# Performance work log

Measured on AMD Instinct MI355X. Metric: run time of the kernel, lower is better.

The kernel has to match this reference:

```python
import jax, jax.numpy as jnp
import numpy as np

EMB_DIM = 1024
NUM_HEADS = 16
HEAD_DIM = EMB_DIM // NUM_HEADS
B, S = 4, 1024


def _split_heads(x):
    # [B, S, E] -> [B, H, S, E/H]
    b, s, e = x.shape
    return x.reshape(b, s, NUM_HEADS, e // NUM_HEADS).transpose(0, 2, 1, 3)


def _merge_heads(x):
    # [B, H, S, D] -> [B, S, H*D]
    b, h, s, d = x.shape
    return x.transpose(0, 2, 1, 3).reshape(b, s, h * d)


def setup_inputs() -> dict:
    key = jax.random.key(0)
    ks = jax.random.split(key, 8)
    w_scale = 0.02
    return {
        "Re": jax.random.normal(ks[0], (B, S, EMB_DIM), jnp.float32),
        "Im": jax.random.normal(ks[1], (B, S, EMB_DIM), jnp.float32),
        "pos_enc": jax.random.normal(ks[2], (B, S, HEAD_DIM), jnp.float32),
        "Wq": jax.random.normal(ks[3], (EMB_DIM, EMB_DIM), jnp.float32) * w_scale,
        "bq": jnp.zeros((EMB_DIM,), jnp.float32),
        "Wk": jax.random.normal(ks[4], (EMB_DIM, EMB_DIM), jnp.float32) * w_scale,
        "bk": jnp.zeros((EMB_DIM,), jnp.float32),
        "Wv": jax.random.normal(ks[5], (EMB_DIM, EMB_DIM), jnp.float32) * w_scale,
        "bv": jnp.zeros((EMB_DIM,), jnp.float32),
        "Wo": jax.random.normal(ks[6], (EMB_DIM, EMB_DIM), jnp.float32) * w_scale,
        "bo": jnp.zeros((EMB_DIM,), jnp.float32),
    }


def reference(Re, Im, pos_enc, Wq, bq, Wk, bk, Wv, bv, Wo, bo):
    # projections + head split
    Q = _split_heads(Re @ Wq + bq)          # [B,H,S,D]
    K = _split_heads(Re @ Wk + bk)          # [B,H,S,D]
    ImH = _split_heads(Im)                  # [B,H,S,D]
    P = pos_enc[:, None, :, :]              # [B,1,S,D] broadcast over heads
    Q = Q + P
    K = K + P
    # real part of (Q + i*Im)(K - i*Im)^T = Q K^T + Im Im^T
    denom = jnp.sqrt(jnp.asarray(EMB_DIM, Q.dtype))  # NOTE: sqrt(emb_dim), as in source
    scores = (jnp.einsum("bhqd,bhkd->bhqk", Q, K)
              + jnp.einsum("bhqd,bhkd->bhqk", ImH, ImH)) / denom
    weights = jax.nn.softmax(scores, axis=-1)
    V = _split_heads(Re @ Wv + bv) + P      # value_pos_enc=True
    out = jnp.einsum("bhqk,bhkd->bhqd", weights, V)
    return _merge_heads(out) @ Wo + bo
```

## Files before the change

### kernel.cpp

```cpp
#include <hip/hip_runtime.h>
#include <hip/hip_bf16.h>
#include <stdint.h>

#define BATCH 4
#define SEQ   1024
#define EMB   1024
#define NHEAD 16
#define HDIM  64
#define MTOT  (BATCH*SEQ)
#define MELEM (MTOT*EMB)

typedef __attribute__((ext_vector_type(8))) short short8;
typedef __attribute__((ext_vector_type(4))) float f32x4;
typedef __attribute__((ext_vector_type(4))) unsigned short us4;

static __device__ __forceinline__ unsigned short f2bf_fast(float f) {
  unsigned u = __builtin_bit_cast(unsigned, f);
  return (unsigned short)((u + 0x8000u) >> 16);
}

static __device__ __forceinline__ void cp16(const void* g, const void* lds_uniform) {
  __builtin_amdgcn_global_load_lds(
      (const __attribute__((address_space(1))) unsigned int*)(uintptr_t)g,
      (__attribute__((address_space(3))) unsigned int*)(unsigned int)(uintptr_t)lds_uniform,
      16, 0, 0);
}

__global__ __launch_bounds__(256) void cvt_bf16(const float* __restrict__ in0,
                                                const float* __restrict__ in1,
                                                short* __restrict__ out0,
                                                short* __restrict__ out1) {
  const float* in  = blockIdx.y ? in1  : in0;
  short*       out = blockIdx.y ? out1 : out0;
  int i = blockIdx.x * 256 + threadIdx.x;
  float4 f = ((const float4*)in)[i];
  unsigned r0 = ((unsigned)f2bf_fast(f.y) << 16) | f2bf_fast(f.x);
  unsigned r1 = ((unsigned)f2bf_fast(f.w) << 16) | f2bf_fast(f.z);
  ((uint2*)out)[i] = make_uint2(r0, r1);
}

__global__ __launch_bounds__(256) void wtrans(const float* __restrict__ W0,
                                              const float* __restrict__ W1,
                                              const float* __restrict__ W2,
                                              const float* __restrict__ W3,
                                              short* __restrict__ WtBase) {
  const int z = blockIdx.z;
  const float* W = (z == 0) ? W0 : (z == 1) ? W1 : (z == 2) ? W2 : W3;
  short* Wt = WtBase + (size_t)z * EMB * EMB;
  __shared__ short tile[32][33];
  int nT = blockIdx.x * 32, kT = blockIdx.y * 32;
  int tx = threadIdx.x, ty = threadIdx.y;
  #pragma unroll
  for (int i = 0; i < 4; ++i)
    tile[ty + 8*i][tx] = (short)f2bf_fast(W[(size_t)(kT + ty + 8*i) * EMB + nT + tx]);
  __syncthreads();
  #pragma unroll
  for (int i = 0; i < 4; ++i)
    Wt[(size_t)(nT + ty + 8*i) * EMB + kT + tx] = tile[tx][ty + 8*i];
}

__global__ __launch_bounds__(256) void gemm_qkv(const short* __restrict__ A,
                                                const short* __restrict__ Wt,
                                                const float* __restrict__ bq,
                                                const float* __restrict__ bk,
                                                const float* __restrict__ bv,
                                                const float* __restrict__ pos,
                                                short* __restrict__ QKbase,
                                                short* __restrict__ vtOut) {
  const int m0 = blockIdx.y * 128, n0 = blockIdx.x * 64;
  const int z = n0 >> 10;
  const float* bias = (z == 0) ? bq : (z == 1 ? bk : bv);

  __shared__ __align__(16) short As[128 * 64];
  __shared__ __align__(16) short Bs[64 * 64];

  const int t = threadIdx.x;
  const int lane = t & 63, w = t >> 6;
  const int wm = w >> 1, wn = w & 1;
  const int quad = lane >> 4, l16 = lane & 15;
  const int lrow8 = lane >> 3, lchunk = lane & 7;
  const int gch = lchunk ^ lrow8;
  const int sw7 = l16 & 7;

  const short* Arow = A  + (size_t)(m0 + w * 32 + lrow8) * EMB + gch * 8;
  const short* Brow = Wt + (size_t)(n0 + w * 16 + lrow8) * EMB + gch * 8;

  f32x4 acc[4][2] = {};

  for (int k0 = 0; k0 < EMB; k0 += 64) {
    #pragma unroll
    for (int s = 0; s < 4; ++s)
      cp16(Arow + (size_t)(s * 8) * EMB + k0, &As[(w * 32 + s * 8) * 64]);
    #pragma unroll
    for (int s = 0; s < 2; ++s)
      cp16(Brow + (size_t)(s * 8) * EMB + k0, &Bs[(w * 16 + s * 8) * 64]);
    __syncthreads();
    #pragma unroll
    for (int ks = 0; ks < 2; ++ks) {
      const int chv = ((ks << 2) + quad) ^ sw7;
      short8 af[4], bfr[2];
      #pragma unroll
      for (int i = 0; i < 4; ++i)
        af[i] = *(const short8*)&As[(wm * 64 + i * 16 + l16) * 64 + chv * 8];
      #pragma unroll
      for (int j = 0; j < 2; ++j)
        bfr[j] = *(const short8*)&Bs[(wn * 32 + j * 16 + l16) * 64 + chv * 8];
      #pragma unroll
      for (int i = 0; i < 4; ++i)
        #pragma unroll
        for (int j = 0; j < 2; ++j)
          acc[i][j] = __builtin_amdgcn_mfma_f32_16x16x32_bf16(af[i], bfr[j], acc[i][j], 0, 0, 0);
    }
    __syncthreads();
  }

  #pragma unroll
  for (int i = 0; i < 4; ++i) {
    int mbase = m0 + wm * 64 + i * 16 + quad * 4;
    #pragma unroll
    for (int j = 0; j < 2; ++j) {
      int n = n0 + wn * 32 + j * 16 + l16;
      int nl = n & 1023;
      float bn = bias[nl];
      int d = nl & (HDIM - 1);
      if (z == 2) {
        int bh = (mbase >> 10) * NHEAD + (nl >> 6);
        int s = mbase & (SEQ - 1);
        us4 pk;
        #pragma unroll
        for (int r = 0; r < 4; ++r) {
          float v = acc[i][j][r] + bn + pos[(size_t)(mbase + r) * HDIM + d];
          pk[r] = f2bf_fast(v);
        }
        *(us4*)&vtOut[((size_t)bh * HDIM + d) * SEQ + s] = pk;
      } else {
        #pragma unroll
        for (int r = 0; r < 4; ++r) {
          int mm = mbase + r;
          float v = acc[i][j][r] + bn + pos[(size_t)mm * HDIM + d];
          QKbase[(size_t)z * MELEM + (size_t)mm * EMB + nl] = (short)f2bf_fast(v);
        }
      }
    }
  }
}

__global__ __launch_bounds__(256) void gemm_wo(const short* __restrict__ A,
                                               const short* __restrict__ Bt,
                                               const float* __restrict__ bias,
                                               float* __restrict__ out) {
  const int m0 = blockIdx.y * 64, n0 = blockIdx.x * 64;

  __shared__ __align__(16) short As[64 * 64];
  __shared__ __align__(16) short Bs[64 * 64];

  const int t = threadIdx.x;
  const int lane = t & 63, w = t >> 6;
  const int wm = w >> 1, wn = w & 1;
  const int quad = lane >> 4, l16 = lane & 15;
  const int lrow8 = lane >> 3, lchunk = lane & 7;
  const int gch = lchunk ^ lrow8;
  const int sw7 = l16 & 7;

  const short* Arow = A  + (size_t)(m0 + w * 16 + lrow8) * EMB + gch * 8;
  const short* Brow = Bt + (size_t)(n0 + w * 16 + lrow8) * EMB + gch * 8;

  f32x4 acc[2][2] = {};

  for (int k0 = 0; k0 < EMB; k0 += 64) {
    #pragma unroll
    for (int s = 0; s < 2; ++s) {
      cp16(Arow + (size_t)(s * 8) * EMB + k0, &As[(w * 16 + s * 8) * 64]);
      cp16(Brow + (size_t)(s * 8) * EMB + k0, &Bs[(w * 16 + s * 8) * 64]);
    }
    __syncthreads();
    #pragma unroll
    for (int ks = 0; ks < 2; ++ks) {
      const int chv = ((ks << 2) + quad) ^ sw7;
      short8 af[2], bfr[2];
      #pragma unroll
      for (int i = 0; i < 2; ++i)
        af[i] = *(const short8*)&As[(wm * 32 + i * 16 + l16) * 64 + chv * 8];
      #pragma unroll
      for (int j = 0; j < 2; ++j)
        bfr[j] = *(const short8*)&Bs[(wn * 32 + j * 16 + l16) * 64 + chv * 8];
      #pragma unroll
      for (int i = 0; i < 2; ++i)
        #pragma unroll
        for (int j = 0; j < 2; ++j)
          acc[i][j] = __builtin_amdgcn_mfma_f32_16x16x32_bf16(af[i], bfr[j], acc[i][j], 0, 0, 0);
    }
    __syncthreads();
  }

  #pragma unroll
  for (int i = 0; i < 2; ++i) {
    int mbase = m0 + wm * 32 + i * 16 + quad * 4;
    #pragma unroll
    for (int j = 0; j < 2; ++j) {
      int n = n0 + wn * 32 + j * 16 + l16;
      float bn = bias[n];
      #pragma unroll
      for (int r = 0; r < 4; ++r)
        out[(size_t)(mbase + r) * EMB + n] = acc[i][j][r] + bn;
    }
  }
}

__global__ __launch_bounds__(256) void attn(const short* __restrict__ Qp,
                                            const short* __restrict__ Kp,
                                            const short* __restrict__ VtG,
                                            const short* __restrict__ Imb,
                                            short* __restrict__ attnA) {
  const int qb = blockIdx.y * 64;
  const int bh = blockIdx.x;
  const int b = bh >> 4, h = bh & 15;
  const int t = threadIdx.x, lane = t & 63, w = t >> 6;
  const int quad = lane >> 4, l16 = lane & 15;
  const int lrow8 = lane >> 3, lchunk = lane & 7;
  const int gch = lchunk ^ lrow8;
  const int sw7 = l16 & 7;

  __shared__ __align__(16) short tiles[3 * 64 * 64];
  __shared__ __align__(16) short Pw[4 * 16 * 64];

  const int q = qb + w * 16 + l16;
  const size_t qoff = ((size_t)(b * SEQ + q)) * EMB + h * HDIM + quad * 8;
  short8 aq[2], aim[2];
  aq[0]  = *(const short8*)&Qp [qoff];
  aq[1]  = *(const short8*)&Qp [qoff + 32];
  aim[0] = *(const short8*)&Imb[qoff];
  aim[1] = *(const short8*)&Imb[qoff + 32];

  float lr[4] = {0.f, 0.f, 0.f, 0.f};
  f32x4 o[4] = {};

  const float SC = 0.03125f * 1.44269504089f;
  const size_t kimBase = ((size_t)b * SEQ) * EMB + h * HDIM + gch * 8;
  const size_t vtBase  = ((size_t)bh * HDIM) * SEQ + gch * 8;

  #pragma unroll
  for (int s = 0; s < 6; ++s) {
    const int I = w * 6 + s;
    const int tz = I >> 3;
    const int row = ((I & 7) * 8) + lrow8;
    const short* g;
    if (tz == 0)      g = Kp  + kimBase + (size_t)row * EMB;
    else if (tz == 1) g = Imb + kimBase + (size_t)row * EMB;
    else              g = VtG + vtBase + (size_t)row * SEQ;
    cp16(g, &tiles[I * 512]);
  }
  __syncthreads();

  for (int kt = 0; kt < 16; ++kt) {
    const int kBaseN = (kt + 1) * 64;

    f32x4 sa[4] = {};
    #pragma unroll
    for (int c = 0; c < 4; ++c) {
      const int rowoff = (c * 16 + l16) * 64;
      #pragma unroll
      for (int st = 0; st < 2; ++st) {
        const int chv = (((st << 2) + quad) ^ sw7) * 8;
        short8 bk = *(const short8*)&tiles[rowoff + chv];
        short8 bi = *(const short8*)&tiles[4096 + rowoff + chv];
        sa[c] = __builtin_amdgcn_mfma_f32_16x16x32_bf16(aq [st], bk, sa[c], 0, 0, 0);
        sa[c] = __builtin_amdgcn_mfma_f32_16x16x32_bf16(aim[st], bi, sa[c], 0, 0, 0);
      }
    }

    __syncthreads();

    if (kt != 15) {
      #pragma unroll
      for (int s = 0; s < 4; ++s) {
        const int I = w * 4 + s;
        const int row = ((I & 7) * 8) + lrow8;
        const short* g = ((I >> 3) ? Imb : Kp) + kimBase + (size_t)(kBaseN + row) * EMB;
        cp16(g, &tiles[I * 512]);
      }
    }

    short* pw = &Pw[w * 1024];
    #pragma unroll
    for (int c = 0; c < 4; ++c) {
      #pragma unroll
      for (int r = 0; r < 4; ++r) {
        float p = __builtin_amdgcn_exp2f(sa[c][r] * SC);
        lr[r] += p;
        const int row = quad * 4 + r;
        const int sch = ((c * 2 + (l16 >> 3)) ^ (row & 7));
        pw[row * 64 + sch * 8 + (l16 & 7)] = (short)f2bf_fast(p);
      }
    }
    short8 ap[2];
    ap[0] = *(const short8*)&pw[l16 * 64 + ((quad       ^ sw7) * 8)];
    ap[1] = *(const short8*)&pw[l16 * 64 + (((4 + quad) ^ sw7) * 8)];

    #pragma unroll
    for (int cd = 0; cd < 4; ++cd) {
      const int rowoff = 8192 + (cd * 16 + l16) * 64;
      #pragma unroll
      for (int st = 0; st < 2; ++st) {
        short8 bv2 = *(const short8*)&tiles[rowoff + (((st << 2) + quad) ^ sw7) * 8];
        o[cd] = __builtin_amdgcn_mfma_f32_16x16x32_bf16(ap[st], bv2, o[cd], 0, 0, 0);
      }
    }

    __syncthreads();

    if (kt != 15) {
      #pragma unroll
      for (int s = 0; s < 2; ++s) {
        const int I = 16 + w * 2 + s;
        const int row = ((I & 7) * 8) + lrow8;
        cp16(VtG + vtBase + (size_t)row * SEQ + kBaseN, &tiles[I * 512]);
      }
    }
  }

  #pragma unroll
  for (int r = 0; r < 4; ++r) {
    #pragma unroll
    for (int msk = 1; msk < 16; msk <<= 1) lr[r] += __shfl_xor(lr[r], msk);
  }
  #pragma unroll
  for (int r = 0; r < 4; ++r) {
    int qq = qb + w * 16 + quad * 4 + r;
    float inv = 1.f / lr[r];
    size_t base = ((size_t)(b * SEQ + qq)) * EMB + h * HDIM;
    #pragma unroll
    for (int cd = 0; cd < 4; ++cd)
      attnA[base + cd * 16 + l16] = (short)f2bf_fast(o[cd][r] * inv);
  }
}

extern "C" void kernel_launch(void* const* d_in, const int* in_sizes, int n_in,
                              void* d_out, int out_size, void* d_ws, size_t ws_size,
                              hipStream_t stream) {
  const float* Re  = (const float*)d_in[0];
  const float* Im  = (const float*)d_in[1];
  const float* pos = (const float*)d_in[2];
  const float* Wq  = (const float*)d_in[3];
  const float* bq  = (const float*)d_in[4];
  const float* Wk  = (const float*)d_in[5];
  const float* bk  = (const float*)d_in[6];
  const float* Wv  = (const float*)d_in[7];
  const float* bv  = (const float*)d_in[8];
  const float* Wo  = (const float*)d_in[9];
  const float* bo  = (const float*)d_in[10];

  short* ws    = (short*)d_ws;
  short* Rebf  = ws;
  short* Imbf  = ws + (size_t)MELEM;
  short* Wt    = ws + (size_t)2 * MELEM;
  short* Qp    = ws + (size_t)3 * MELEM;
  short* Kp    = Qp + (size_t)MELEM;
  short* VtG   = Qp + (size_t)2 * MELEM;
  short* attnA = ws + (size_t)6 * MELEM;

  cvt_bf16<<<dim3(MELEM / 1024, 2), 256, 0, stream>>>(Re, Im, Rebf, Imbf);

  wtrans<<<dim3(32, 32, 4), dim3(32, 8), 0, stream>>>(Wq, Wk, Wv, Wo, Wt);

  gemm_qkv<<<dim3(3 * EMB / 64, MTOT / 128), 256, 0, stream>>>(
      Rebf, Wt, bq, bk, bv, pos, Qp, VtG);

  attn<<<dim3(BATCH * NHEAD, SEQ / 64), 256, 0, stream>>>(
      Qp, Kp, VtG, Imbf, attnA);

  gemm_wo<<<dim3(EMB / 64, MTOT / 64), 256, 0, stream>>>(
      attnA, Wt + 3 * EMB * EMB, bo, (float*)d_out);
}
```

Before: 202.4 us.

## Split attention warps 2x2 over query and key halves for operand reuse

Reorganizes the attention kernel so each of the four waves handles 32 queries by 32 keys instead of 16 queries by 64 keys. Each K/Im/V fragment read from LDS is now reused across two query groups, which halves the LDS operand reads per MFMA. The cost is an extra barrier per iteration to share the probability tile, plus a cross-wave reduction of partial outputs and row sums through LDS at the end. It also adds a launch-bounds occupancy hint.

After: 214.0 us. 5.7% more time.

```diff
diff --git a/kernel.cpp b/kernel.cpp
--- a/kernel.cpp
+++ b/kernel.cpp
@@ -207,11 +207,11 @@
   }
 }
 
-__global__ __launch_bounds__(256) void attn(const short* __restrict__ Qp,
-                                            const short* __restrict__ Kp,
-                                            const short* __restrict__ VtG,
-                                            const short* __restrict__ Imb,
-                                            short* __restrict__ attnA) {
+__global__ __launch_bounds__(256, 4) void attn(const short* __restrict__ Qp,
+                                               const short* __restrict__ Kp,
+                                               const short* __restrict__ VtG,
+                                               const short* __restrict__ Imb,
+                                               short* __restrict__ attnA) {
   const int qb = blockIdx.y * 64;
   const int bh = blockIdx.x;
   const int b = bh >> 4, h = bh & 15;
@@ -220,20 +220,25 @@
   const int lrow8 = lane >> 3, lchunk = lane & 7;
   const int gch = lchunk ^ lrow8;
   const int sw7 = l16 & 7;
+  const int qh = w >> 1;
+  const int kh = w & 1;
 
   __shared__ __align__(16) short tiles[3 * 64 * 64];
-  __shared__ __align__(16) short Pw[4 * 16 * 64];
-
-  const int q = qb + w * 16 + l16;
-  const size_t qoff = ((size_t)(b * SEQ + q)) * EMB + h * HDIM + quad * 8;
-  short8 aq[2], aim[2];
-  aq[0]  = *(const short8*)&Qp [qoff];
-  aq[1]  = *(const short8*)&Qp [qoff + 32];
-  aim[0] = *(const short8*)&Imb[qoff];
-  aim[1] = *(const short8*)&Imb[qoff + 32];
-
-  float lr[4] = {0.f, 0.f, 0.f, 0.f};
-  f32x4 o[4] = {};
+  __shared__ __align__(16) short Pw[64 * 64];
+
+  short8 aq[2][2], aim[2][2];
+  #pragma unroll
+  for (int qg = 0; qg < 2; ++qg) {
+    const int q = qb + qh * 32 + qg * 16 + l16;
+    const size_t qoff = ((size_t)(b * SEQ + q)) * EMB + h * HDIM + quad * 8;
+    aq [qg][0] = *(const short8*)&Qp [qoff];
+    aq [qg][1] = *(const short8*)&Qp [qoff + 32];
+    aim[qg][0] = *(const short8*)&Imb[qoff];
+    aim[qg][1] = *(const short8*)&Imb[qoff + 32];
+  }
+
+  float lr[2][4] = {};
+  f32x4 o[2][4] = {};
 
   const float SC = 0.03125f * 1.44269504089f;
   const size_t kimBase = ((size_t)b * SEQ) * EMB + h * HDIM + gch * 8;
@@ -255,17 +260,20 @@
   for (int kt = 0; kt < 16; ++kt) {
     const int kBaseN = (kt + 1) * 64;
 
-    f32x4 sa[4] = {};
-    #pragma unroll
-    for (int c = 0; c < 4; ++c) {
-      const int rowoff = (c * 16 + l16) * 64;
+    f32x4 sa[2][2] = {};
+    #pragma unroll
+    for (int kg = 0; kg < 2; ++kg) {
+      const int rowoff = (kh * 32 + kg * 16 + l16) * 64;
       #pragma unroll
       for (int st = 0; st < 2; ++st) {
         const int chv = (((st << 2) + quad) ^ sw7) * 8;
         short8 bk = *(const short8*)&tiles[rowoff + chv];
         short8 bi = *(const short8*)&tiles[4096 + rowoff + chv];
-        sa[c] = __builtin_amdgcn_mfma_f32_16x16x32_bf16(aq [st], bk, sa[c], 0, 0, 0);
-        sa[c] = __builtin_amdgcn_mfma_f32_16x16x32_bf16(aim[st], bi, sa[c], 0, 0, 0);
+        #pragma unroll
+        for (int qg = 0; qg < 2; ++qg) {
+          sa[qg][kg] = __builtin_amdgcn_mfma_f32_16x16x32_bf16(aq [qg][st], bk, sa[qg][kg], 0, 0, 0);
+          sa[qg][kg] = __builtin_amdgcn_mfma_f32_16x16x32_bf16(aim[qg][st], bi, sa[qg][kg], 0, 0, 0);
+        }
       }
     }
 
@@ -281,30 +289,33 @@
       }
     }
 
-    short* pw = &Pw[w * 1024];
-    #pragma unroll
-    for (int c = 0; c < 4; ++c) {
-      #pragma unroll
-      for (int r = 0; r < 4; ++r) {
-        float p = __builtin_amdgcn_exp2f(sa[c][r] * SC);
-        lr[r] += p;
-        const int row = quad * 4 + r;
-        const int sch = ((c * 2 + (l16 >> 3)) ^ (row & 7));
-        pw[row * 64 + sch * 8 + (l16 & 7)] = (short)f2bf_fast(p);
-      }
-    }
+    #pragma unroll
+    for (int qg = 0; qg < 2; ++qg)
+      #pragma unroll
+      for (int kg = 0; kg < 2; ++kg)
+        #pragma unroll
+        for (int r = 0; r < 4; ++r) {
+          float p = __builtin_amdgcn_exp2f(sa[qg][kg][r] * SC);
+          lr[qg][r] += p;
+          const int row = qh * 32 + qg * 16 + quad * 4 + r;
+          const int sch = (kh * 4 + kg * 2 + (l16 >> 3)) ^ ((quad * 4 + r) & 7);
+          Pw[row * 64 + sch * 8 + (l16 & 7)] = (short)f2bf_fast(p);
+        }
+
+    __asm__ __volatile__("s_waitcnt lgkmcnt(0)\n\ts_barrier" ::: "memory");
+
     short8 ap[2];
-    ap[0] = *(const short8*)&pw[l16 * 64 + ((quad       ^ sw7) * 8)];
-    ap[1] = *(const short8*)&pw[l16 * 64 + (((4 + quad) ^ sw7) * 8)];
-
+    #pragma unroll
+    for (int qg2 = 0; qg2 < 2; ++qg2)
+      ap[qg2] = *(const short8*)&Pw[(qh * 32 + qg2 * 16 + l16) * 64 +
+                                    (((kh * 4 + quad) ^ sw7) * 8)];
     #pragma unroll
     for (int cd = 0; cd < 4; ++cd) {
-      const int rowoff = 8192 + (cd * 16 + l16) * 64;
-      #pragma unroll
-      for (int st = 0; st < 2; ++st) {
-        short8 bv2 = *(const short8*)&tiles[rowoff + (((st << 2) + quad) ^ sw7) * 8];
-        o[cd] = __builtin_amdgcn_mfma_f32_16x16x32_bf16(ap[st], bv2, o[cd], 0, 0, 0);
-      }
+      short8 bv2 = *(const short8*)&tiles[8192 + (cd * 16 + l16) * 64 +
+                                          (((kh * 4 + quad) ^ sw7) * 8)];
+      #pragma unroll
+      for (int qg2 = 0; qg2 < 2; ++qg2)
+        o[qg2][cd] = __builtin_amdgcn_mfma_f32_16x16x32_bf16(ap[qg2], bv2, o[qg2][cd], 0, 0, 0);
     }
 
     __syncthreads();
@@ -319,19 +330,41 @@
     }
   }
 
-  #pragma unroll
-  for (int r = 0; r < 4; ++r) {
-    #pragma unroll
-    for (int msk = 1; msk < 16; msk <<= 1) lr[r] += __shfl_xor(lr[r], msk);
-  }
-  #pragma unroll
-  for (int r = 0; r < 4; ++r) {
-    int qq = qb + w * 16 + quad * 4 + r;
-    float inv = 1.f / lr[r];
-    size_t base = ((size_t)(b * SEQ + qq)) * EMB + h * HDIM;
-    #pragma unroll
-    for (int cd = 0; cd < 4; ++cd)
-      attnA[base + cd * 16 + l16] = (short)f2bf_fast(o[cd][r] * inv);
+  float* lbuf = (float*)Pw;
+  #pragma unroll
+  for (int qg = 0; qg < 2; ++qg)
+    #pragma unroll
+    for (int r = 0; r < 4; ++r) {
+      float s = lr[qg][r];
+      #pragma unroll
+      for (int msk = 1; msk < 16; msk <<= 1) s += __shfl_xor(s, msk);
+      if (l16 == 0) lbuf[(qh * 32 + qg * 16 + quad * 4 + r) * 2 + kh] = s;
+    }
+  float* fbuf = (float*)tiles;
+  if (kh == 1) {
+    #pragma unroll
+    for (int qg2 = 0; qg2 < 2; ++qg2)
+      #pragma unroll
+      for (int cd = 0; cd < 4; ++cd)
+        #pragma unroll
+        for (int r = 0; r < 4; ++r)
+          fbuf[(size_t)(qh * 32 + qg2 * 16 + quad * 4 + r) * 65 + cd * 16 + l16] = o[qg2][cd][r];
+  }
+  __syncthreads();
+  if (kh == 0) {
+    #pragma unroll
+    for (int qg2 = 0; qg2 < 2; ++qg2)
+      #pragma unroll
+      for (int r = 0; r < 4; ++r) {
+        const int row = qh * 32 + qg2 * 16 + quad * 4 + r;
+        float linv = 1.f / (lbuf[row * 2] + lbuf[row * 2 + 1]);
+        size_t base = ((size_t)(b * SEQ + qb + row)) * EMB + h * HDIM;
+        #pragma unroll
+        for (int cd = 0; cd < 4; ++cd) {
+          float v = (o[qg2][cd][r] + fbuf[(size_t)row * 65 + cd * 16 + l16]) * linv;
+          attnA[base + cd * 16 + l16] = (short)f2bf_fast(v);
+        }
+      }
   }
 }
 
```

## Double-buffer LDS tiles in QKV and Wo GEMMs with k-step 32 prefetch

Applied to the files above, without the earlier changes.

Both projection GEMMs switch from single-buffered 64-wide K tiles to double-buffered 32-wide K tiles. The global-to-LDS copy for the next slice is issued before the MFMAs on the current slice, and the loop is fully unrolled. The XOR swizzle is reworked for the 32-column layout. This is meant to overlap global load latency with compute, at the cost of twice as many barriers and shorter MFMA runs between them.

New measurement: 217.9 us. 7.7% more time.

```diff
diff --git a/kernel.cpp b/kernel.cpp
--- a/kernel.cpp
+++ b/kernel.cpp
@@ -71,47 +71,53 @@
   const int z = n0 >> 10;
   const float* bias = (z == 0) ? bq : (z == 1 ? bk : bv);
 
-  __shared__ __align__(16) short As[128 * 64];
-  __shared__ __align__(16) short Bs[64 * 64];
+  __shared__ __align__(16) short As[2][128 * 32];
+  __shared__ __align__(16) short Bs[2][64 * 32];
 
   const int t = threadIdx.x;
   const int lane = t & 63, w = t >> 6;
   const int wm = w >> 1, wn = w & 1;
   const int quad = lane >> 4, l16 = lane & 15;
-  const int lrow8 = lane >> 3, lchunk = lane & 7;
-  const int gch = lchunk ^ lrow8;
-  const int sw7 = l16 & 7;
-
-  const short* Arow = A  + (size_t)(m0 + w * 32 + lrow8) * EMB + gch * 8;
-  const short* Brow = Wt + (size_t)(n0 + w * 16 + lrow8) * EMB + gch * 8;
+  const int lrow4 = lane >> 2;
+  const int gch4 = (lane & 3) ^ ((lane >> 3) & 3);
+  const int sch = (quad ^ ((l16 >> 1) & 3)) * 8;
+
+  const short* A0 = A  + (size_t)(m0 + (w * 2 + 0) * 16 + lrow4) * EMB + gch4 * 8;
+  const short* A1 = A  + (size_t)(m0 + (w * 2 + 1) * 16 + lrow4) * EMB + gch4 * 8;
+  const short* B0 = Wt + (size_t)(n0 + w * 16 + lrow4) * EMB + gch4 * 8;
 
   f32x4 acc[4][2] = {};
 
-  for (int k0 = 0; k0 < EMB; k0 += 64) {
-    #pragma unroll
-    for (int s = 0; s < 4; ++s)
-      cp16(Arow + (size_t)(s * 8) * EMB + k0, &As[(w * 32 + s * 8) * 64]);
-    #pragma unroll
-    for (int s = 0; s < 2; ++s)
-      cp16(Brow + (size_t)(s * 8) * EMB + k0, &Bs[(w * 16 + s * 8) * 64]);
-    __syncthreads();
-    #pragma unroll
-    for (int ks = 0; ks < 2; ++ks) {
-      const int chv = ((ks << 2) + quad) ^ sw7;
+  cp16(A0, &As[0][(w * 2 + 0) * 512]);
+  cp16(A1, &As[0][(w * 2 + 1) * 512]);
+  cp16(B0, &Bs[0][w * 512]);
+  __syncthreads();
+
+  #pragma unroll
+  for (int cc = 0; cc < 16; ++cc) {
+    #pragma unroll
+    for (int half = 0; half < 2; ++half) {
+      const int c = cc * 2 + half;
+      const int nk = (c + 1) * 32;
+      if (c < 31) {
+        cp16(A0 + nk, &As[1 - half][(w * 2 + 0) * 512]);
+        cp16(A1 + nk, &As[1 - half][(w * 2 + 1) * 512]);
+        cp16(B0 + nk, &Bs[1 - half][w * 512]);
+      }
       short8 af[4], bfr[2];
       #pragma unroll
       for (int i = 0; i < 4; ++i)
-        af[i] = *(const short8*)&As[(wm * 64 + i * 16 + l16) * 64 + chv * 8];
+        af[i] = *(const short8*)&As[half][(wm * 64 + i * 16 + l16) * 32 + sch];
       #pragma unroll
       for (int j = 0; j < 2; ++j)
-        bfr[j] = *(const short8*)&Bs[(wn * 32 + j * 16 + l16) * 64 + chv * 8];
+        bfr[j] = *(const short8*)&Bs[half][(wn * 32 + j * 16 + l16) * 32 + sch];
       #pragma unroll
       for (int i = 0; i < 4; ++i)
         #pragma unroll
         for (int j = 0; j < 2; ++j)
           acc[i][j] = __builtin_amdgcn_mfma_f32_16x16x32_bf16(af[i], bfr[j], acc[i][j], 0, 0, 0);
-    }
-    __syncthreads();
+      __syncthreads();
+    }
   }
 
   #pragma unroll
@@ -151,46 +157,50 @@
                                                float* __restrict__ out) {
   const int m0 = blockIdx.y * 64, n0 = blockIdx.x * 64;
 
-  __shared__ __align__(16) short As[64 * 64];
-  __shared__ __align__(16) short Bs[64 * 64];
+  __shared__ __align__(16) short As[2][64 * 32];
+  __shared__ __align__(16) short Bs[2][64 * 32];
 
   const int t = threadIdx.x;
   const int lane = t & 63, w = t >> 6;
   const int wm = w >> 1, wn = w & 1;
   const int quad = lane >> 4, l16 = lane & 15;
-  const int lrow8 = lane >> 3, lchunk = lane & 7;
-  const int gch = lchunk ^ lrow8;
-  const int sw7 = l16 & 7;
-
-  const short* Arow = A  + (size_t)(m0 + w * 16 + lrow8) * EMB + gch * 8;
-  const short* Brow = Bt + (size_t)(n0 + w * 16 + lrow8) * EMB + gch * 8;
+  const int lrow4 = lane >> 2;
+  const int gch4 = (lane & 3) ^ ((lane >> 3) & 3);
+  const int sch = (quad ^ ((l16 >> 1) & 3)) * 8;
+
+  const short* A0 = A  + (size_t)(m0 + w * 16 + lrow4) * EMB + gch4 * 8;
+  const short* B0 = Bt + (size_t)(n0 + w * 16 + lrow4) * EMB + gch4 * 8;
 
   f32x4 acc[2][2] = {};
 
-  for (int k0 = 0; k0 < EMB; k0 += 64) {
-    #pragma unroll
-    for (int s = 0; s < 2; ++s) {
-      cp16(Arow + (size_t)(s * 8) * EMB + k0, &As[(w * 16 + s * 8) * 64]);
-      cp16(Brow + (size_t)(s * 8) * EMB + k0, &Bs[(w * 16 + s * 8) * 64]);
-    }
-    __syncthreads();
-    #pragma unroll
-    for (int ks = 0; ks < 2; ++ks) {
-      const int chv = ((ks << 2) + quad) ^ sw7;
+  cp16(A0, &As[0][w * 512]);
+  cp16(B0, &Bs[0][w * 512]);
+  __syncthreads();
+
+  #pragma unroll
+  for (int cc = 0; cc < 16; ++cc) {
+    #pragma unroll
+    for (int half = 0; half < 2; ++half) {
+      const int c = cc * 2 + half;
+      const int nk = (c + 1) * 32;
+      if (c < 31) {
+        cp16(A0 + nk, &As[1 - half][w * 512]);
+        cp16(B0 + nk, &Bs[1 - half][w * 512]);
+      }
       short8 af[2], bfr[2];
       #pragma unroll
       for (int i = 0; i < 2; ++i)
-        af[i] = *(const short8*)&As[(wm * 32 + i * 16 + l16) * 64 + chv * 8];
+        af[i] = *(const short8*)&As[half][(wm * 32 + i * 16 + l16) * 32 + sch];
       #pragma unroll
       for (int j = 0; j < 2; ++j)
-        bfr[j] = *(const short8*)&Bs[(wn * 32 + j * 16 + l16) * 64 + chv * 8];
+        bfr[j] = *(const short8*)&Bs[half][(wn * 32 + j * 16 + l16) * 32 + sch];
       #pragma unroll
       for (int i = 0; i < 2; ++i)
         #pragma unroll
         for (int j = 0; j < 2; ++j)
           acc[i][j] = __builtin_amdgcn_mfma_f32_16x16x32_bf16(af[i], bfr[j], acc[i][j], 0, 0, 0);
-    }
-    __syncthreads();
+      __syncthreads();
+    }
   }
 
   #pragma unroll
@@ -289,8 +299,8 @@
         float p = __builtin_amdgcn_exp2f(sa[c][r] * SC);
         lr[r] += p;
         const int row = quad * 4 + r;
-        const int sch = ((c * 2 + (l16 >> 3)) ^ (row & 7));
-        pw[row * 64 + sch * 8 + (l16 & 7)] = (short)f2bf_fast(p);
+        const int sch2 = ((c * 2 + (l16 >> 3)) ^ (row & 7));
+        pw[row * 64 + sch2 * 8 + (l16 & 7)] = (short)f2bf_fast(p);
       }
     }
     short8 ap[2];
```
